# Performance work log

Measured on AMD Instinct MI355X. Metric: run time of the kernel, lower is better.

Reference implementation:

```python
import jax, jax.numpy as jnp
import numpy as np

TOP_K = 4
ALPHA = 1.702
LIMIT = 7.0


def setup_inputs() -> dict:
    key = jax.random.key(0)
    ks = jax.random.split(key, 7)
    B, S, H, I, E = 1, 512, 2880, 2880, 16
    s = 0.02
    return {
        "hidden_states": jax.random.normal(ks[0], (B, S, H), dtype=jnp.float32),
        "router_w": jax.random.normal(ks[1], (H, E), dtype=jnp.float32) * s,
        "router_b": jax.random.normal(ks[2], (E,), dtype=jnp.float32) * s,
        "gate_up_w": jax.random.normal(ks[3], (E, H, 2 * I), dtype=jnp.float32) * s,
        "gate_up_b": jax.random.normal(ks[4], (E, 2 * I), dtype=jnp.float32) * s,
        "down_w": jax.random.normal(ks[5], (E, I, H), dtype=jnp.float32) * s,
        "down_b": jax.random.normal(ks[6], (E, H), dtype=jnp.float32) * s,
    }


def reference(hidden_states, router_w, router_b, gate_up_w, gate_up_b, down_w, down_b):
    B, S, H = hidden_states.shape
    x = hidden_states.reshape(-1, H)                      # [T, H]
    T = x.shape[0]

    # Router: top-k + softmax over selected logits, scattered back to [T, E]
    router_logits = x @ router_w + router_b               # [T, E]
    top_v, top_i = jax.lax.top_k(router_logits, TOP_K)    # [T, K]
    top_v = jax.nn.softmax(top_v, axis=-1)
    router_scores = jnp.zeros_like(router_logits).at[
        jnp.arange(T)[:, None], top_i
    ].set(top_v)                                          # [T, E]

    # Dense all-experts GLU (matches the repeat-across-experts formulation)
    gate_up = jnp.einsum('th,ehd->etd', x, gate_up_w) + gate_up_b[:, None, :]  # [E, T, 2I]
    gate = gate_up[..., ::2]                              # [E, T, I]
    up = gate_up[..., 1::2]                               # [E, T, I]
    gate = jnp.minimum(gate, LIMIT)
    up = jnp.clip(up, -LIMIT, LIMIT)
    glu = gate * jax.nn.sigmoid(gate * ALPHA)
    expert_out = jnp.einsum('eti,eih->eth', (up + 1.0) * glu, down_w) + down_b[:, None, :]  # [E, T, H]

    # Masked combine with routing weights
    out = jnp.sum(expert_out * router_scores.T[:, :, None], axis=0)  # [T, H]
    return (out.reshape(B, S, H),)
```

## Files before the change

kernel.cpp:

```cpp
#include <hip/hip_runtime.h>
#include <hip/hip_bf16.h>

#define NTOK 512
#define HDIM 2880
#define NGU  5760
#define NEXP 16
#define KSTEPS 90
#define MT 160
#define MFR 10

typedef float  f32x4  __attribute__((ext_vector_type(4)));
typedef float  f32x2  __attribute__((ext_vector_type(2)));
typedef short  bf16x8 __attribute__((ext_vector_type(8)));

__device__ __forceinline__ unsigned short f2bf(float f) {
  union { float f; unsigned u; } a; a.f = f;
  unsigned r = a.u + 0x7FFFu + ((a.u >> 16) & 1u);
  return (unsigned short)(r >> 16);
}

__device__ __forceinline__ void lds_barrier() {
  asm volatile("s_waitcnt lgkmcnt(0)" ::: "memory");
  __builtin_amdgcn_s_barrier();
  asm volatile("" ::: "memory");
}


__global__ __launch_bounds__(256) void k_router(
    const float* __restrict__ x, const float* __restrict__ rw,
    const float* __restrict__ rb, int* __restrict__ counts,
    int* __restrict__ top_e, float* __restrict__ top_w)
{
  const int t = blockIdx.x;
  const int tid = threadIdx.x;
  __shared__ float red[256][17];
  float acc[NEXP];
#pragma unroll
  for (int e = 0; e < NEXP; ++e) acc[e] = 0.f;
  const float* xr = x + (size_t)t * HDIM;
  for (int h = tid; h < HDIM; h += 256) {
    float xv = xr[h];
    const f32x4* wr = (const f32x4*)(rw + (size_t)h * NEXP);
#pragma unroll
    for (int q = 0; q < 4; ++q) {
      f32x4 w = wr[q];
#pragma unroll
      for (int j = 0; j < 4; ++j) acc[q*4+j] += xv * w[j];
    }
  }
#pragma unroll
  for (int e = 0; e < NEXP; ++e) red[tid][e] = acc[e];
  __syncthreads();
  for (int s = 128; s > 0; s >>= 1) {
    if (tid < s) {
#pragma unroll
      for (int e = 0; e < NEXP; ++e) red[tid][e] += red[tid + s][e];
    }
    __syncthreads();
  }
  if (tid == 0) {
    float v[NEXP];
#pragma unroll
    for (int e = 0; e < NEXP; ++e) v[e] = red[0][e] + rb[e];
    int mask = 0; float tv[4]; int ti[4];
    for (int k = 0; k < 4; ++k) {
      float best = -3.4e38f; int bi = 0;
      for (int e = 0; e < NEXP; ++e)
        if (!((mask >> e) & 1) && v[e] > best) { best = v[e]; bi = e; }
      mask |= 1 << bi; tv[k] = best; ti[k] = bi;
    }
    float s = 0.f, ex[4];
    for (int k = 0; k < 4; ++k) { ex[k] = __expf(tv[k] - tv[0]); s += ex[k]; }
    float inv = 1.f / s;
    for (int k = 0; k < 4; ++k) {
      top_e[t*4+k] = ti[k];
      top_w[t*4+k] = ex[k] * inv;
      atomicAdd(&counts[ti[k]], 1);
    }
  }
}

__global__ __launch_bounds__(64) void k_fill(
    const int* __restrict__ top_e, const float* __restrict__ top_w,
    const int* __restrict__ counts, int* __restrict__ seg,
    int* __restrict__ pair_tok, float* __restrict__ pair_w,
    int* __restrict__ pair_of)
{
  const int e = blockIdx.x;
  const int lane = threadIdx.x;
  int base = 0;
  for (int i = 0; i < e; ++i) base += counts[i];
  if (lane == 0) {
    seg[e] = base;
    if (e == NEXP - 1) seg[NEXP] = base + counts[e];
  }
  for (int t0 = 0; t0 < NTOK; t0 += 64) {
    int t = t0 + lane;
    int my = -1;
#pragma unroll
    for (int k = 0; k < 4; ++k) if (top_e[t*4+k] == e) my = k;
    unsigned long long m = __ballot(my >= 0);
    if (my >= 0) {
      int pre = __popcll(m & ((1ull << lane) - 1ull));
      pair_tok[base + pre] = t;
      pair_w[base + pre] = top_w[t*4+my];
      pair_of[t*4 + my] = base + pre;
    }
    base += (int)__popcll(m);
  }
}

__global__ __launch_bounds__(256) void k_xbf16(
    const float* __restrict__ x, unsigned short* __restrict__ xb,
    int* __restrict__ counts)
{
  if (blockIdx.x == 0 && threadIdx.x < NEXP) counts[threadIdx.x] = 0;
  int i = (blockIdx.x * 256 + threadIdx.x) * 8;
  f32x4 a = *(const f32x4*)(x + i);
  f32x4 b = *(const f32x4*)(x + i + 4);
  bf16x8 o;
#pragma unroll
  for (int j = 0; j < 4; ++j) { o[j] = (short)f2bf(a[j]); o[4+j] = (short)f2bf(b[j]); }
  *(bf16x8*)(xb + i) = o;
}

__global__ __launch_bounds__(256, 2) void k_gateup(
    const unsigned short* __restrict__ xb, const float* __restrict__ gw,
    const float* __restrict__ gb, const int* __restrict__ seg,
    const int* __restrict__ pair_tok, const float* __restrict__ pair_w,
    unsigned short* __restrict__ act)
{
  const int e = blockIdx.z;
  const int segs = seg[e];
  const int n_e = seg[e+1] - segs;
  const int m0 = blockIdx.y * MT;
  if (m0 >= n_e) return;
  const int tid = threadIdx.x;
  const int lane = tid & 63;
  const int wid = tid >> 6;
  const int l15 = lane & 15, lg = lane >> 4;
  const int fcb = blockIdx.x * 128 + wid * 32;
  const int fcE = fcb + 2*l15;
  const int colf = min(2*fcb + 4*l15, NGU - 4);

  __shared__ unsigned short Alds[2][MT][40];

  const float* Bq = gw + (size_t)e * HDIM * NGU + colf + (size_t)lg * 8 * NGU;

  const unsigned short* sp0 = nullptr;
  const unsigned short* sp1 = nullptr;
  const int r0 = tid >> 1, h0 = tid & 1;
  const int r1 = (tid + 256) >> 1, h1 = tid & 1;
  if (m0 + r0 < n_e) sp0 = xb + (size_t)pair_tok[segs + m0 + r0] * HDIM + h0*16;
  if (tid < 2*MT - 256 && m0 + r1 < n_e)
    sp1 = xb + (size_t)pair_tok[segs + m0 + r1] * HDIM + h1*16;

  f32x4 accgE[MFR], accuE[MFR], accgO[MFR], accuO[MFR];
  {
    f32x4 b = __builtin_nontemporal_load((const f32x4*)(gb + (size_t)e * NGU + colf));
#pragma unroll
    for (int m = 0; m < MFR; ++m)
#pragma unroll
      for (int r = 0; r < 4; ++r) {
        accgE[m][r] = b[0]; accuE[m][r] = b[1];
        accgO[m][r] = b[2]; accuO[m][r] = b[3];
      }
  }

  auto stage = [&](int ks, int b) {
    bf16x8 z = {0,0,0,0,0,0,0,0};
    bf16x8 v0 = z, v1 = z;
    if (sp0) { v0 = *(const bf16x8*)(sp0 + ks*32); v1 = *(const bf16x8*)(sp0 + ks*32 + 8); }
    *(bf16x8*)&Alds[b][r0][h0*16]     = v0;
    *(bf16x8*)&Alds[b][r0][h0*16 + 8] = v1;
    if (tid < 2*MT - 256) {
      bf16x8 w0 = z, w1 = z;
      if (sp1) { w0 = *(const bf16x8*)(sp1 + ks*32); w1 = *(const bf16x8*)(sp1 + ks*32 + 8); }
      *(bf16x8*)&Alds[b][r1][h1*16]     = w0;
      *(bf16x8*)&Alds[b][r1][h1*16 + 8] = w1;
    }
  };

  f32x4 bA[8];
  auto loadB = [&](int ks) {
    const float* bp = Bq + (size_t)ks * 32 * NGU;
#pragma unroll
    for (int j = 0; j < 8; ++j)
      bA[j] = __builtin_nontemporal_load((const f32x4*)(bp + (size_t)j * NGU));
  };

  loadB(0);
  stage(0, 0);
  lds_barrier();
  int buf = 0;

  for (int ks = 0; ks < KSTEPS; ++ks) {
    if (ks + 1 < KSTEPS) stage(ks + 1, buf ^ 1);
    bf16x8 bgE, buE, bgO, buO;
#pragma unroll
    for (int j = 0; j < 8; ++j) {
      bgE[j] = (short)f2bf(bA[j][0]); buE[j] = (short)f2bf(bA[j][1]);
      bgO[j] = (short)f2bf(bA[j][2]); buO[j] = (short)f2bf(bA[j][3]);
    }
    if (ks + 1 < KSTEPS) loadB(ks + 1);
#pragma unroll
    for (int m = 0; m < MFR; ++m) {
      bf16x8 a = *(const bf16x8*)&Alds[buf][m*16 + l15][lg*8];
      accgE[m] = __builtin_amdgcn_mfma_f32_16x16x32_bf16(a, bgE, accgE[m], 0, 0, 0);
      accuE[m] = __builtin_amdgcn_mfma_f32_16x16x32_bf16(a, buE, accuE[m], 0, 0, 0);
      accgO[m] = __builtin_amdgcn_mfma_f32_16x16x32_bf16(a, bgO, accgO[m], 0, 0, 0);
      accuO[m] = __builtin_amdgcn_mfma_f32_16x16x32_bf16(a, buO, accuO[m], 0, 0, 0);
    }
    lds_barrier();
    buf ^= 1;
  }

  if (fcE < HDIM) {
#pragma unroll
    for (int m = 0; m < MFR; ++m) {
#pragma unroll
      for (int r = 0; r < 4; ++r) {
        int grow = m0 + m*16 + lg*4 + r;
        if (grow < n_e) {
          float pw = pair_w[segs + grow];
          float gE = fminf(accgE[m][r], 7.f);
          float uE = fminf(fmaxf(accuE[m][r], -7.f), 7.f);
          float avE = (uE + 1.f) * (gE / (1.f + __expf(-1.702f * gE))) * pw;
          float gO = fminf(accgO[m][r], 7.f);
          float uO = fminf(fmaxf(accuO[m][r], -7.f), 7.f);
          float avO = (uO + 1.f) * (gO / (1.f + __expf(-1.702f * gO))) * pw;
          unsigned pk = (unsigned)f2bf(avE) | ((unsigned)f2bf(avO) << 16);
          *(unsigned*)&act[(size_t)(segs + grow) * HDIM + fcE] = pk;
        }
      }
    }
  }
}

__global__ __launch_bounds__(256, 3) void k_down(
    const unsigned short* __restrict__ act, const float* __restrict__ dw,
    const int* __restrict__ seg, const int* __restrict__ pair_tok,
    float* __restrict__ partial)
{
  const int e = blockIdx.z;
  const int segs = seg[e];
  const int n_e = seg[e+1] - segs;
  const int m0 = blockIdx.y * MT;
  if (m0 >= n_e) return;
  const int tid = threadIdx.x;
  const int lane = tid & 63;
  const int wid = tid >> 6;
  const int l15 = lane & 15, lg = lane >> 4;
  const int cb = blockIdx.x * 128 + wid * 32;
  const int cE = cb + 2*l15;
  const int colc = min(cE, HDIM - 2);

  __shared__ unsigned short Alds[2][MT][40];

  const float* Bq = dw + (size_t)e * HDIM * HDIM + colc + (size_t)lg * 8 * HDIM;

  const unsigned short* sp0 = nullptr;
  const unsigned short* sp1 = nullptr;
  const int r0 = tid >> 1, h0 = tid & 1;
  const int r1 = (tid + 256) >> 1, h1 = tid & 1;
  if (m0 + r0 < n_e) sp0 = act + (size_t)(segs + m0 + r0) * HDIM + h0*16;
  if (tid < 2*MT - 256 && m0 + r1 < n_e)
    sp1 = act + (size_t)(segs + m0 + r1) * HDIM + h1*16;

  f32x4 accE[MFR], accO[MFR];
#pragma unroll
  for (int m = 0; m < MFR; ++m)
#pragma unroll
    for (int r = 0; r < 4; ++r) { accE[m][r] = 0.f; accO[m][r] = 0.f; }

  auto stage = [&](int ks, int b) {
    bf16x8 z = {0,0,0,0,0,0,0,0};
    bf16x8 v0 = z, v1 = z;
    if (sp0) { v0 = *(const bf16x8*)(sp0 + ks*32); v1 = *(const bf16x8*)(sp0 + ks*32 + 8); }
    *(bf16x8*)&Alds[b][r0][h0*16]     = v0;
    *(bf16x8*)&Alds[b][r0][h0*16 + 8] = v1;
    if (tid < 2*MT - 256) {
      bf16x8 w0 = z, w1 = z;
      if (sp1) { w0 = *(const bf16x8*)(sp1 + ks*32); w1 = *(const bf16x8*)(sp1 + ks*32 + 8); }
      *(bf16x8*)&Alds[b][r1][h1*16]     = w0;
      *(bf16x8*)&Alds[b][r1][h1*16 + 8] = w1;
    }
  };

  f32x2 bA[8];
  auto loadB = [&](int ks) {
    const float* bp = Bq + (size_t)ks * 32 * HDIM;
#pragma unroll
    for (int j = 0; j < 8; ++j)
      bA[j] = __builtin_nontemporal_load((const f32x2*)(bp + (size_t)j * HDIM));
  };

  loadB(0);
  stage(0, 0);
  lds_barrier();
  int buf = 0;

  for (int ks = 0; ks < KSTEPS; ++ks) {
    if (ks + 1 < KSTEPS) stage(ks + 1, buf ^ 1);
    bf16x8 bfE, bfO;
#pragma unroll
    for (int j = 0; j < 8; ++j) { bfE[j] = (short)f2bf(bA[j][0]); bfO[j] = (short)f2bf(bA[j][1]); }
    if (ks + 1 < KSTEPS) loadB(ks + 1);
#pragma unroll
    for (int m = 0; m < MFR; ++m) {
      bf16x8 a = *(const bf16x8*)&Alds[buf][m*16 + l15][lg*8];
      accE[m] = __builtin_amdgcn_mfma_f32_16x16x32_bf16(a, bfE, accE[m], 0, 0, 0);
      accO[m] = __builtin_amdgcn_mfma_f32_16x16x32_bf16(a, bfO, accO[m], 0, 0, 0);
    }
    lds_barrier();
    buf ^= 1;
  }

  if (cE < HDIM) {
#pragma unroll
    for (int m = 0; m < MFR; ++m) {
#pragma unroll
      for (int r = 0; r < 4; ++r) {
        int grow = m0 + m*16 + lg*4 + r;
        if (grow < n_e) {
          f32x2 v = { accE[m][r], accO[m][r] };
          *(f32x2*)&partial[(size_t)(segs + grow) * HDIM + cE] = v;
        }
      }
    }
  }
}

__global__ __launch_bounds__(256) void k_gather(
    const float* __restrict__ partial, const int* __restrict__ pair_of,
    const int* __restrict__ top_e, const float* __restrict__ top_w,
    const float* __restrict__ db, float* __restrict__ out)
{
  const int t = blockIdx.x;
  const int tid = threadIdx.x;
  const int p0 = pair_of[t*4+0], p1 = pair_of[t*4+1];
  const int p2 = pair_of[t*4+2], p3 = pair_of[t*4+3];
  const float w0 = top_w[t*4+0], w1 = top_w[t*4+1];
  const float w2 = top_w[t*4+2], w3 = top_w[t*4+3];
  const float* r0 = partial + (size_t)p0 * HDIM;
  const float* r1 = partial + (size_t)p1 * HDIM;
  const float* r2 = partial + (size_t)p2 * HDIM;
  const float* r3 = partial + (size_t)p3 * HDIM;
  const float* b0 = db + (size_t)top_e[t*4+0] * HDIM;
  const float* b1 = db + (size_t)top_e[t*4+1] * HDIM;
  const float* b2 = db + (size_t)top_e[t*4+2] * HDIM;
  const float* b3 = db + (size_t)top_e[t*4+3] * HDIM;
  float* o = out + (size_t)t * HDIM;
  for (int p = tid; p < HDIM/4; p += 256) {
    f32x4 v0 = *(const f32x4*)(r0 + 4*p);
    f32x4 v1 = *(const f32x4*)(r1 + 4*p);
    f32x4 v2 = *(const f32x4*)(r2 + 4*p);
    f32x4 v3 = *(const f32x4*)(r3 + 4*p);
    f32x4 c0 = *(const f32x4*)(b0 + 4*p);
    f32x4 c1 = *(const f32x4*)(b1 + 4*p);
    f32x4 c2 = *(const f32x4*)(b2 + 4*p);
    f32x4 c3 = *(const f32x4*)(b3 + 4*p);
    f32x4 s;
#pragma unroll
    for (int j = 0; j < 4; ++j)
      s[j] = (v0[j] + v1[j]) + (v2[j] + v3[j])
           + (w0*c0[j] + w1*c1[j]) + (w2*c2[j] + w3*c3[j]);
    *(f32x4*)(o + 4*p) = s;
  }
}


extern "C" void kernel_launch(void* const* d_in, const int* in_sizes, int n_in,
                              void* d_out, int out_size, void* d_ws, size_t ws_size,
                              hipStream_t stream) {
  const float* x  = (const float*)d_in[0];
  const float* rw = (const float*)d_in[1];
  const float* rb = (const float*)d_in[2];
  const float* gw = (const float*)d_in[3];
  const float* gb = (const float*)d_in[4];
  const float* dw = (const float*)d_in[5];
  const float* db = (const float*)d_in[6];
  float* out = (float*)d_out;

  char* w = (char*)d_ws;
  int*   counts   = (int*)(w);
  int*   seg      = (int*)(w + 64);
  int*   top_e    = (int*)(w + 1024);
  float* top_w    = (float*)(w + 1024 + 8192);
  int*   pair_tok = (int*)(w + 1024 + 16384);
  float* pair_w   = (float*)(w + 1024 + 24576);
  int*   pair_of  = (int*)(w + 1024 + 32768);
  unsigned short* xb  = (unsigned short*)(w + (1 << 20));
  unsigned short* act = (unsigned short*)(w + (8 << 20));
  float* partial = (float*)(w + (64ull << 20));

  k_xbf16<<<(NTOK*HDIM)/(256*8), 256, 0, stream>>>(x, xb, counts);
  k_router<<<NTOK, 256, 0, stream>>>(x, rw, rb, counts, top_e, top_w);
  k_fill<<<NEXP, 64, 0, stream>>>(top_e, top_w, counts, seg, pair_tok, pair_w, pair_of);

  dim3 gg(23, 2, NEXP);
  k_gateup<<<gg, 256, 0, stream>>>(xb, gw, gb, seg, pair_tok, pair_w, act);

  dim3 gd(23, 2, NEXP);
  k_down<<<gd, 256, 0, stream>>>(act, dw, seg, pair_tok, partial);

  k_gather<<<NTOK, 256, 0, stream>>>(partial, pair_of, top_e, top_w, db, out);
}
```

Baseline: 447.4 us.

## Split down-projection K dimension in two and reduce halves in gather

The down-projection kernel now splits its reduction dimension into two halves, each handled by a separate block writing to its own partial buffer, doubling the grid's y dimension. The gather kernel sums both partial buffers before applying routing weights and bias. This is meant to raise the number of concurrent blocks and improve occupancy and memory-level parallelism for the weight-streaming down GEMM. The cost is a second partial buffer and extra reads in the gather step.

```diff
diff --git a/kernel.cpp b/kernel.cpp
--- a/kernel.cpp
+++ b/kernel.cpp
@@ -6,8 +6,10 @@
 #define NGU  5760
 #define NEXP 16
 #define KSTEPS 90
+#define KSH   45
 #define MT 160
 #define MFR 10
+#define PARTELT ((size_t)(NTOK*4) * HDIM)
 
 typedef float  f32x4  __attribute__((ext_vector_type(4)));
 typedef float  f32x2  __attribute__((ext_vector_type(2)));
@@ -243,9 +245,11 @@
     float* __restrict__ partial)
 {
   const int e = blockIdx.z;
+  const int mi = blockIdx.y >> 1;
+  const int kh = blockIdx.y & 1;
   const int segs = seg[e];
   const int n_e = seg[e+1] - segs;
-  const int m0 = blockIdx.y * MT;
+  const int m0 = mi * MT;
   if (m0 >= n_e) return;
   const int tid = threadIdx.x;
   const int lane = tid & 63;
@@ -254,18 +258,21 @@
   const int cb = blockIdx.x * 128 + wid * 32;
   const int cE = cb + 2*l15;
   const int colc = min(cE, HDIM - 2);
+  const int k0 = kh * (KSH * 32);
 
   __shared__ unsigned short Alds[2][MT][40];
 
-  const float* Bq = dw + (size_t)e * HDIM * HDIM + colc + (size_t)lg * 8 * HDIM;
+  float* po = partial + (size_t)kh * PARTELT;
+  const float* Bq = dw + (size_t)e * HDIM * HDIM + colc
+                  + (size_t)(k0 + lg * 8) * HDIM;
 
   const unsigned short* sp0 = nullptr;
   const unsigned short* sp1 = nullptr;
   const int r0 = tid >> 1, h0 = tid & 1;
   const int r1 = (tid + 256) >> 1, h1 = tid & 1;
-  if (m0 + r0 < n_e) sp0 = act + (size_t)(segs + m0 + r0) * HDIM + h0*16;
+  if (m0 + r0 < n_e) sp0 = act + (size_t)(segs + m0 + r0) * HDIM + k0 + h0*16;
   if (tid < 2*MT - 256 && m0 + r1 < n_e)
-    sp1 = act + (size_t)(segs + m0 + r1) * HDIM + h1*16;
+    sp1 = act + (size_t)(segs + m0 + r1) * HDIM + k0 + h1*16;
 
   f32x4 accE[MFR], accO[MFR];
 #pragma unroll
@@ -300,12 +307,12 @@
   lds_barrier();
   int buf = 0;
 
-  for (int ks = 0; ks < KSTEPS; ++ks) {
-    if (ks + 1 < KSTEPS) stage(ks + 1, buf ^ 1);
+  for (int ks = 0; ks < KSH; ++ks) {
+    if (ks + 1 < KSH) stage(ks + 1, buf ^ 1);
     bf16x8 bfE, bfO;
 #pragma unroll
     for (int j = 0; j < 8; ++j) { bfE[j] = (short)f2bf(bA[j][0]); bfO[j] = (short)f2bf(bA[j][1]); }
-    if (ks + 1 < KSTEPS) loadB(ks + 1);
+    if (ks + 1 < KSH) loadB(ks + 1);
 #pragma unroll
     for (int m = 0; m < MFR; ++m) {
       bf16x8 a = *(const bf16x8*)&Alds[buf][m*16 + l15][lg*8];
@@ -324,7 +331,7 @@
         int grow = m0 + m*16 + lg*4 + r;
         if (grow < n_e) {
           f32x2 v = { accE[m][r], accO[m][r] };
-          *(f32x2*)&partial[(size_t)(segs + grow) * HDIM + cE] = v;
+          *(f32x2*)&po[(size_t)(segs + grow) * HDIM + cE] = v;
         }
       }
     }
@@ -346,6 +353,10 @@
   const float* r1 = partial + (size_t)p1 * HDIM;
   const float* r2 = partial + (size_t)p2 * HDIM;
   const float* r3 = partial + (size_t)p3 * HDIM;
+  const float* q0 = r0 + PARTELT;
+  const float* q1 = r1 + PARTELT;
+  const float* q2 = r2 + PARTELT;
+  const float* q3 = r3 + PARTELT;
   const float* b0 = db + (size_t)top_e[t*4+0] * HDIM;
   const float* b1 = db + (size_t)top_e[t*4+1] * HDIM;
   const float* b2 = db + (size_t)top_e[t*4+2] * HDIM;
@@ -356,6 +367,10 @@
     f32x4 v1 = *(const f32x4*)(r1 + 4*p);
     f32x4 v2 = *(const f32x4*)(r2 + 4*p);
     f32x4 v3 = *(const f32x4*)(r3 + 4*p);
+    f32x4 u0 = *(const f32x4*)(q0 + 4*p);
+    f32x4 u1 = *(const f32x4*)(q1 + 4*p);
+    f32x4 u2 = *(const f32x4*)(q2 + 4*p);
+    f32x4 u3 = *(const f32x4*)(q3 + 4*p);
     f32x4 c0 = *(const f32x4*)(b0 + 4*p);
     f32x4 c1 = *(const f32x4*)(b1 + 4*p);
     f32x4 c2 = *(const f32x4*)(b2 + 4*p);
@@ -363,7 +378,8 @@
     f32x4 s;
 #pragma unroll
     for (int j = 0; j < 4; ++j)
-      s[j] = (v0[j] + v1[j]) + (v2[j] + v3[j])
+      s[j] = ((v0[j] + u0[j]) + (v1[j] + u1[j]))
+           + ((v2[j] + u2[j]) + (v3[j] + u3[j]))
            + (w0*c0[j] + w1*c1[j]) + (w2*c2[j] + w3*c3[j]);
     *(f32x4*)(o + 4*p) = s;
   }
@@ -401,7 +417,7 @@
   dim3 gg(23, 2, NEXP);
   k_gateup<<<gg, 256, 0, stream>>>(xb, gw, gb, seg, pair_tok, pair_w, act);
 
-  dim3 gd(23, 2, NEXP);
+  dim3 gd(23, 4, NEXP);
   k_down<<<gd, 256, 0, stream>>>(act, dw, seg, pair_tok, partial);
 
   k_gather<<<NTOK, 256, 0, stream>>>(partial, pair_of, top_e, top_w, db, out);
```

After: 437.5 us. 2.2% less time.
